# Kernel tuning notes

Hardware: AMD Instinct MI355X
Metric: run time of the kernel (lower is better)

Reference implementation:

```python
import jax, jax.numpy as jnp
import numpy as np

N, IN_C, OUT_C = 8192, 256, 256


def setup_inputs() -> dict:
    key = jax.random.key(0)
    ks = jax.random.split(key, 12)
    p = lambda k, shape: (jax.random.normal(k, shape, jnp.float32) * 0.05)
    return {
        "X": jax.random.normal(ks[0], (IN_C,), jnp.float32),
        "head": 100,
        "tail": 7,
        "E": jax.random.uniform(ks[1], (N, N), jnp.float32),
        "H": jax.random.normal(ks[2], (N, OUT_C), jnp.float32),
        "W_x_z": p(ks[3], (IN_C, OUT_C)),
        "W_h_z": p(ks[4], (OUT_C, OUT_C)),
        "conv_z": p(ks[5], (OUT_C, OUT_C)),
        "b_z": jnp.zeros((1, OUT_C), jnp.float32),
        "W_x_r": p(ks[6], (IN_C, OUT_C)),
        "W_h_r": p(ks[7], (OUT_C, OUT_C)),
        "conv_r": p(ks[8], (OUT_C, OUT_C)),
        "b_r": jnp.zeros((1, OUT_C), jnp.float32),
        "W_x_h": p(ks[9], (IN_C, OUT_C)),
        "W_h_h": p(ks[10], (OUT_C, OUT_C)),
        "b_h": jnp.zeros((1, OUT_C), jnp.float32),
    }


def reference(X, head, tail, E, H, W_x_z, W_h_z, conv_z, b_z,
              W_x_r, W_h_r, conv_r, b_r, W_x_h, W_h_h, b_h):
    # --- edge-weight update ---
    # Original: M = 0.5*I with M[head,tail]=0.5; Ep = E with Ep[head,tail]+=1;
    # E_new = M @ Ep.  M@Ep scales every row by 0.5 and (if head!=tail) adds
    # 0.5*Ep[tail] into row `head`.  Same math, O(N^2) instead of O(N^3).
    Ep = E.at[head, tail].add(1.0)
    E_new = 0.5 * Ep
    if head != tail:  # head/tail are Python ints (static)
        E_new = E_new.at[head].add(0.5 * Ep[tail])

    h_head = H[head]                 # [OUT_C]
    agg = E_new[head] @ H            # GCN aggregation over neighbors: [OUT_C]

    Z = jax.nn.sigmoid(X @ W_x_z + h_head @ W_h_z + agg @ conv_z + b_z[0])
    R = jax.nn.sigmoid(X @ W_x_r + h_head @ W_h_r + agg @ conv_r + b_r[0])
    H_tilde = jnp.tanh(X @ W_x_h + (h_head * R) @ W_h_h + b_h[0])

    H_new = H.at[head].set(Z * h_head + (1.0 - Z) * H_tilde)
    return E_new, H_new
```

## Files before the change

kernel.cpp:

```cpp
#include <hip/hip_runtime.h>
#include <math.h>

#define NN 8192
#define CC 256
#define LOG2N 13

typedef float f32x4 __attribute__((ext_vector_type(4)));

#define WS_AGGP 0
#define WS_ZRP  32768
#define WS_HTP  38912

__global__ void k_agg_partial(const float* __restrict__ E, const float* __restrict__ H,
                              const int* __restrict__ dh, const int* __restrict__ dt,
                              float* __restrict__ aggP) {
    __shared__ float e_sh[64];
    const int head = dh[0], tail = dt[0];
    const int i0 = blockIdx.x * 64;
    const int t = threadIdx.x;
    if (t < 64) {
        const int i = i0 + t;
        float e = 0.5f * E[(size_t)head * NN + i];
        if (head != tail) e += 0.5f * E[(size_t)tail * NN + i];
        if (i == tail) e += 0.5f;
        e_sh[t] = e;
    }
    __syncthreads();
    float acc = 0.f;
    for (int k = 0; k < 64; ++k)
        acc += e_sh[k] * H[(size_t)(i0 + k) * CC + t];
    aggP[blockIdx.x * CC + t] = acc;
}

__global__ void k_zr_partial(const float* __restrict__ X, const float* __restrict__ H,
                             const int* __restrict__ dh,
                             const float* __restrict__ Wxz, const float* __restrict__ Whz,
                             const float* __restrict__ Cz,  const float* __restrict__ Wxr,
                             const float* __restrict__ Whr, const float* __restrict__ Cr,
                             const float* __restrict__ aggP, float* __restrict__ zrP) {
    __shared__ float v_sh[64];
    const int m = blockIdx.x >> 2, q = blockIdx.x & 3;
    const int t = threadIdx.x;
    const int head = dh[0];
    const float* W;
    switch (m) {
        case 0: W = Wxz; break; case 1: W = Whz; break; case 2: W = Cz; break;
        case 3: W = Wxr; break; case 4: W = Whr; break; default: W = Cr; break;
    }
    if (t < 64) {
        const int k = q * 64 + t;
        float v;
        if (m == 0 || m == 3)      v = X[k];
        else if (m == 1 || m == 4) v = H[(size_t)head * CC + k];
        else { v = 0.f; for (int b = 0; b < 128; ++b) v += aggP[b * CC + k]; }
        v_sh[t] = v;
    }
    __syncthreads();
    float acc = 0.f;
    for (int kk = 0; kk < 64; ++kk)
        acc += v_sh[kk] * W[(size_t)(q * 64 + kk) * CC + t];
    zrP[(m * 4 + q) * CC + t] = acc;
}

__global__ void k_ht_partial(const float* __restrict__ X, const float* __restrict__ H,
                             const int* __restrict__ dh, const float* __restrict__ br,
                             const float* __restrict__ zrP,
                             const float* __restrict__ Wxh, const float* __restrict__ Whh,
                             float* __restrict__ htP) {
    __shared__ float v_sh[64];
    const int m = blockIdx.x >> 2, q = blockIdx.x & 3;
    const int t = threadIdx.x;
    if (t < 64) {
        const int k = q * 64 + t;
        if (m == 0) {
            v_sh[t] = X[k];
        } else {
            float sr = br[k];
            for (int p = 12; p < 24; ++p) sr += zrP[p * CC + k];
            const float r = 1.f / (1.f + expf(-sr));
            v_sh[t] = H[(size_t)dh[0] * CC + k] * r;
        }
    }
    __syncthreads();
    const float* W = m ? Whh : Wxh;
    float acc = 0.f;
    for (int kk = 0; kk < 64; ++kk)
        acc += v_sh[kk] * W[(size_t)(q * 64 + kk) * CC + t];
    htP[(m * 4 + q) * CC + t] = acc;
}

__global__ void __launch_bounds__(256) k_big(
        const float* __restrict__ E, const float* __restrict__ H,
        const int* __restrict__ dh, const int* __restrict__ dt,
        const float* __restrict__ bz, const float* __restrict__ bh,
        const float* __restrict__ zrP, const float* __restrict__ htP,
        float* __restrict__ out) {
    const int head = dh[0], tail = dt[0];
    const size_t nn = (size_t)NN * NN;

    if (blockIdx.x == gridDim.x - 1) {
        const int c = threadIdx.x;
        float sz = bz[c];
        for (int p = 0; p < 12; ++p) sz += zrP[p * CC + c];
        const float z = 1.f / (1.f + expf(-sz));
        float s = bh[c];
        for (int p = 0; p < 8; ++p) s += htP[p * CC + c];
        const float ht = tanhf(s);
        const float h = H[(size_t)head * CC + c];
        out[nn + (size_t)head * CC + c] = z * h + (1.f - z) * ht;
    }

    const size_t total4 = (nn + (size_t)NN * CC) >> 2;
    const size_t stride = (size_t)gridDim.x * blockDim.x;
    for (size_t idx = (size_t)blockIdx.x * blockDim.x + threadIdx.x; idx < total4; idx += stride) {
        const size_t e = idx << 2;
        if (e < nn) {
            f32x4 v = __builtin_nontemporal_load((const f32x4*)(E + e));
            f32x4 o = v * 0.5f;
            const int i = (int)(e >> LOG2N);
            if (i == head) {
                const int j = (int)(e & (NN - 1));
                if (head != tail) {
                    const f32x4 w = *(const f32x4*)(E + (size_t)tail * NN + j);
                    o += w * 0.5f;
                }
                if (tail >= j && tail < j + 4) o[tail - j] += 0.5f;
            }
            __builtin_nontemporal_store(o, (f32x4*)(out + e));
        } else {
            const size_t t = e - nn;
            const int row = (int)(t >> 8);
            if (row != head) {
                const f32x4 hv = __builtin_nontemporal_load((const f32x4*)(H + t));
                __builtin_nontemporal_store(hv, (f32x4*)(out + nn + t));
            }
        }
    }
}

extern "C" void kernel_launch(void* const* d_in, const int* in_sizes, int n_in,
                              void* d_out, int out_size, void* d_ws, size_t ws_size,
                              hipStream_t stream) {
    const float* X    = (const float*)d_in[0];
    const int*   dh   = (const int*)d_in[1];
    const int*   dt   = (const int*)d_in[2];
    const float* E    = (const float*)d_in[3];
    const float* H    = (const float*)d_in[4];
    const float* Wxz  = (const float*)d_in[5];
    const float* Whz  = (const float*)d_in[6];
    const float* Cz   = (const float*)d_in[7];
    const float* bz   = (const float*)d_in[8];
    const float* Wxr  = (const float*)d_in[9];
    const float* Whr  = (const float*)d_in[10];
    const float* Cr   = (const float*)d_in[11];
    const float* br   = (const float*)d_in[12];
    const float* Wxh  = (const float*)d_in[13];
    const float* Whh  = (const float*)d_in[14];
    const float* bh   = (const float*)d_in[15];
    float* out = (float*)d_out;
    float* ws  = (float*)d_ws;

    float* aggP = ws + WS_AGGP;
    float* zrP  = ws + WS_ZRP;
    float* htP  = ws + WS_HTP;

    k_agg_partial<<<128, 256, 0, stream>>>(E, H, dh, dt, aggP);
    k_zr_partial<<<24, 256, 0, stream>>>(X, H, dh, Wxz, Whz, Cz, Wxr, Whr, Cr, aggP, zrP);
    k_ht_partial<<<8, 256, 0, stream>>>(X, H, dh, br, zrP, Wxh, Whh, htP);
    k_big<<<2048, 256, 0, stream>>>(E, H, dh, dt, bz, bh, zrP, htP, out);
}
```

Measured before the change: 113.9 us.

## Fold H-tilde matvec into streaming kernel and vectorize aggregation

Removes the separate k_ht_partial launch. The X@W_x_h partials move into the z/r matvec kernel, and block 0 of the big streaming kernel computes R, the (h*R)@W_h_h matvec, and the final head row. The aggregation kernel now reads H with float4 loads spread over four row groups and combines them with a shared-memory reduction. The goal is to save one kernel launch and its serialization, at the cost of one block doing a serial 256-long matvec while the other blocks stream E.

```diff
diff --git a/kernel.cpp b/kernel.cpp
--- a/kernel.cpp
+++ b/kernel.cpp
@@ -9,15 +9,16 @@
 
 #define WS_AGGP 0
 #define WS_ZRP  32768
-#define WS_HTP  38912
 
-__global__ void k_agg_partial(const float* __restrict__ E, const float* __restrict__ H,
-                              const int* __restrict__ dh, const int* __restrict__ dt,
-                              float* __restrict__ aggP) {
+__global__ void __launch_bounds__(256) k_agg(
+        const float* __restrict__ E, const float* __restrict__ H,
+        const int* __restrict__ dh, const int* __restrict__ dt,
+        float* __restrict__ aggP) {
     __shared__ float e_sh[64];
+    __shared__ f32x4 red[4][64];
     const int head = dh[0], tail = dt[0];
+    const int t = threadIdx.x;
     const int i0 = blockIdx.x * 64;
-    const int t = threadIdx.x;
     if (t < 64) {
         const int i = i0 + t;
         float e = 0.5f * E[(size_t)head * NN + i];
@@ -26,96 +27,96 @@
         e_sh[t] = e;
     }
     __syncthreads();
-    float acc = 0.f;
-    for (int k = 0; k < 64; ++k)
-        acc += e_sh[k] * H[(size_t)(i0 + k) * CC + t];
-    aggP[blockIdx.x * CC + t] = acc;
+    const int g = t >> 6, c = (t & 63) << 2;
+    f32x4 acc = {0.f, 0.f, 0.f, 0.f};
+    #pragma unroll
+    for (int it = 0; it < 16; ++it) {
+        const int r = it * 4 + g;
+        const f32x4 hv = *(const f32x4*)(H + (size_t)(i0 + r) * CC + c);
+        acc += hv * e_sh[r];
+    }
+    red[g][t & 63] = acc;
+    __syncthreads();
+    if (g == 0) {
+        const f32x4 s = red[0][t] + red[1][t] + red[2][t] + red[3][t];
+        *(f32x4*)(aggP + blockIdx.x * CC + (t << 2)) = s;
+    }
 }
 
-__global__ void k_zr_partial(const float* __restrict__ X, const float* __restrict__ H,
-                             const int* __restrict__ dh,
-                             const float* __restrict__ Wxz, const float* __restrict__ Whz,
-                             const float* __restrict__ Cz,  const float* __restrict__ Wxr,
-                             const float* __restrict__ Whr, const float* __restrict__ Cr,
-                             const float* __restrict__ aggP, float* __restrict__ zrP) {
+__global__ void __launch_bounds__(256) k_mv(
+        const float* __restrict__ X, const float* __restrict__ H,
+        const int* __restrict__ dh,
+        const float* __restrict__ Wxz, const float* __restrict__ Whz,
+        const float* __restrict__ Cz,  const float* __restrict__ Wxr,
+        const float* __restrict__ Whr, const float* __restrict__ Cr,
+        const float* __restrict__ Wxh,
+        const float* __restrict__ aggP, float* __restrict__ zrP) {
     __shared__ float v_sh[64];
     const int m = blockIdx.x >> 2, q = blockIdx.x & 3;
     const int t = threadIdx.x;
-    const int head = dh[0];
     const float* W;
     switch (m) {
         case 0: W = Wxz; break; case 1: W = Whz; break; case 2: W = Cz; break;
-        case 3: W = Wxr; break; case 4: W = Whr; break; default: W = Cr; break;
+        case 3: W = Wxr; break; case 4: W = Whr; break; case 5: W = Cr; break;
+        default: W = Wxh; break;
     }
     if (t < 64) {
         const int k = q * 64 + t;
         float v;
-        if (m == 0 || m == 3)      v = X[k];
-        else if (m == 1 || m == 4) v = H[(size_t)head * CC + k];
-        else { v = 0.f; for (int b = 0; b < 128; ++b) v += aggP[b * CC + k]; }
+        if (m == 1 || m == 4)      v = H[(size_t)dh[0] * CC + k];
+        else if (m == 2 || m == 5) { v = 0.f; for (int b = 0; b < 128; ++b) v += aggP[b * CC + k]; }
+        else                       v = X[k];
         v_sh[t] = v;
     }
     __syncthreads();
     float acc = 0.f;
+    #pragma unroll
     for (int kk = 0; kk < 64; ++kk)
         acc += v_sh[kk] * W[(size_t)(q * 64 + kk) * CC + t];
     zrP[(m * 4 + q) * CC + t] = acc;
 }
 
-__global__ void k_ht_partial(const float* __restrict__ X, const float* __restrict__ H,
-                             const int* __restrict__ dh, const float* __restrict__ br,
-                             const float* __restrict__ zrP,
-                             const float* __restrict__ Wxh, const float* __restrict__ Whh,
-                             float* __restrict__ htP) {
-    __shared__ float v_sh[64];
-    const int m = blockIdx.x >> 2, q = blockIdx.x & 3;
-    const int t = threadIdx.x;
-    if (t < 64) {
-        const int k = q * 64 + t;
-        if (m == 0) {
-            v_sh[t] = X[k];
-        } else {
-            float sr = br[k];
-            for (int p = 12; p < 24; ++p) sr += zrP[p * CC + k];
-            const float r = 1.f / (1.f + expf(-sr));
-            v_sh[t] = H[(size_t)dh[0] * CC + k] * r;
-        }
-    }
-    __syncthreads();
-    const float* W = m ? Whh : Wxh;
-    float acc = 0.f;
-    for (int kk = 0; kk < 64; ++kk)
-        acc += v_sh[kk] * W[(size_t)(q * 64 + kk) * CC + t];
-    htP[(m * 4 + q) * CC + t] = acc;
-}
-
 __global__ void __launch_bounds__(256) k_big(
         const float* __restrict__ E, const float* __restrict__ H,
         const int* __restrict__ dh, const int* __restrict__ dt,
-        const float* __restrict__ bz, const float* __restrict__ bh,
-        const float* __restrict__ zrP, const float* __restrict__ htP,
-        float* __restrict__ out) {
+        const float* __restrict__ bz, const float* __restrict__ br,
+        const float* __restrict__ bh, const float* __restrict__ Whh,
+        const float* __restrict__ zrP, float* __restrict__ out) {
     const int head = dh[0], tail = dt[0];
     const size_t nn = (size_t)NN * NN;
 
-    if (blockIdx.x == gridDim.x - 1) {
+    if (blockIdx.x == 0) {
+        __shared__ float rs_sh[CC];
         const int c = threadIdx.x;
-        float sz = bz[c];
-        for (int p = 0; p < 12; ++p) sz += zrP[p * CC + c];
+        float sz = bz[c], sr = br[c];
+        #pragma unroll
+        for (int p = 0; p < 12; ++p)  sz += zrP[p * CC + c];
+        #pragma unroll
+        for (int p = 12; p < 24; ++p) sr += zrP[p * CC + c];
         const float z = 1.f / (1.f + expf(-sz));
-        float s = bh[c];
-        for (int p = 0; p < 8; ++p) s += htP[p * CC + c];
+        const float r = 1.f / (1.f + expf(-sr));
+        const float h = H[(size_t)head * CC + c];
+        rs_sh[c] = h * r;
+        __syncthreads();
+        float acc = 0.f;
+        #pragma unroll 16
+        for (int k = 0; k < CC; ++k)
+            acc += rs_sh[k] * Whh[(size_t)k * CC + c];
+        float s = bh[c] + acc;
+        #pragma unroll
+        for (int p = 24; p < 28; ++p) s += zrP[p * CC + c];
         const float ht = tanhf(s);
-        const float h = H[(size_t)head * CC + c];
         out[nn + (size_t)head * CC + c] = z * h + (1.f - z) * ht;
+        return;
     }
 
     const size_t total4 = (nn + (size_t)NN * CC) >> 2;
-    const size_t stride = (size_t)gridDim.x * blockDim.x;
-    for (size_t idx = (size_t)blockIdx.x * blockDim.x + threadIdx.x; idx < total4; idx += stride) {
+    const size_t nstream = (size_t)(gridDim.x - 1) * blockDim.x;
+    for (size_t idx = (size_t)(blockIdx.x - 1) * blockDim.x + threadIdx.x;
+         idx < total4; idx += nstream) {
         const size_t e = idx << 2;
         if (e < nn) {
-            f32x4 v = __builtin_nontemporal_load((const f32x4*)(E + e));
+            const f32x4 v = __builtin_nontemporal_load((const f32x4*)(E + e));
             f32x4 o = v * 0.5f;
             const int i = (int)(e >> LOG2N);
             if (i == head) {
@@ -128,11 +129,10 @@
             }
             __builtin_nontemporal_store(o, (f32x4*)(out + e));
         } else {
-            const size_t t = e - nn;
-            const int row = (int)(t >> 8);
-            if (row != head) {
-                const f32x4 hv = __builtin_nontemporal_load((const f32x4*)(H + t));
-                __builtin_nontemporal_store(hv, (f32x4*)(out + nn + t));
+            const size_t tt = e - nn;
+            if ((int)(tt >> 8) != head) {
+                const f32x4 hv = __builtin_nontemporal_load((const f32x4*)(H + tt));
+                __builtin_nontemporal_store(hv, (f32x4*)(out + nn + tt));
             }
         }
     }
@@ -162,10 +162,8 @@
 
     float* aggP = ws + WS_AGGP;
     float* zrP  = ws + WS_ZRP;
-    float* htP  = ws + WS_HTP;
 
-    k_agg_partial<<<128, 256, 0, stream>>>(E, H, dh, dt, aggP);
-    k_zr_partial<<<24, 256, 0, stream>>>(X, H, dh, Wxz, Whz, Cz, Wxr, Whr, Cr, aggP, zrP);
-    k_ht_partial<<<8, 256, 0, stream>>>(X, H, dh, br, zrP, Wxh, Whh, htP);
-    k_big<<<2048, 256, 0, stream>>>(E, H, dh, dt, bz, bh, zrP, htP, out);
+    k_agg<<<128, 256, 0, stream>>>(E, H, dh, dt, aggP);
+    k_mv<<<28, 256, 0, stream>>>(X, H, dh, Wxz, Whz, Cz, Wxr, Whr, Cr, Wxh, aggP, zrP);
+    k_big<<<2049, 256, 0, stream>>>(E, H, dh, dt, bz, br, bh, Whh, zrP, out);
 }
```

Result: no change. 114.1 us (+0.1%).
